# Optimization experiments

Measured on AMD Instinct MI355X. Metric: run time of the kernel, lower is better.

The kernel has to match this reference:

```python
import jax, jax.numpy as jnp
import numpy as np
from jax import lax

LATENT_DIM = 512
UNITS = LATENT_DIM // 2  # per-direction LSTM units (Keras LSTM(latent_dim//2))
FEAT = 512


def _lstm_scan(x, W, U, b):
    """Keras-style LSTM over x: [B, T, F]. Gate order i, f, g(candidate), o.
    Returns (hs [B,T,u], h_last [B,u], c_last [B,u])."""
    B = x.shape[0]
    u = U.shape[0]
    # Precompute input projections for all timesteps (one big GEMM).
    xz = jnp.einsum('btf,fg->btg', x, W) + b  # [B, T, 4u]

    def step(carry, zt):
        h, c = carry
        z = zt + h @ U  # [B, 4u]
        i = jax.nn.sigmoid(z[:, :u])
        f = jax.nn.sigmoid(z[:, u:2 * u])
        g = jnp.tanh(z[:, 2 * u:3 * u])
        o = jax.nn.sigmoid(z[:, 3 * u:])
        c_new = f * c + i * g
        h_new = o * jnp.tanh(c_new)
        return (h_new, c_new), h_new

    init = (jnp.zeros((B, u), x.dtype), jnp.zeros((B, u), x.dtype))
    (h_last, c_last), hs = lax.scan(step, init, jnp.swapaxes(xz, 0, 1))
    return jnp.swapaxes(hs, 0, 1), h_last, c_last


def setup_inputs() -> dict:
    key = jax.random.key(0)
    ks = jax.random.split(key, 7)
    B, T, F, u = 64, 1024, FEAT, UNITS
    s_in = 1.0 / np.sqrt(F)
    s_rec = 1.0 / np.sqrt(u)
    return {
        'x': jax.random.normal(ks[0], (B, T, F), jnp.float32),
        'W_fwd': jax.random.normal(ks[1], (F, 4 * u), jnp.float32) * s_in,
        'U_fwd': jax.random.normal(ks[2], (u, 4 * u), jnp.float32) * s_rec,
        'b_fwd': jnp.zeros((4 * u,), jnp.float32),
        'W_bwd': jax.random.normal(ks[3], (F, 4 * u), jnp.float32) * s_in,
        'U_bwd': jax.random.normal(ks[4], (u, 4 * u), jnp.float32) * s_rec,
        'b_bwd': jnp.zeros((4 * u,), jnp.float32),
    }


def reference(x, W_fwd, U_fwd, b_fwd, W_bwd, U_bwd, b_bwd):
    # Forward direction
    hs_f, h_f, c_f = _lstm_scan(x, W_fwd, U_fwd, b_fwd)
    # Backward direction: process reversed sequence, re-reverse outputs (Keras Bidirectional)
    hs_b, h_b, c_b = _lstm_scan(x[:, ::-1, :], W_bwd, U_bwd, b_bwd)
    hs_b = hs_b[:, ::-1, :]
    enc_out = jnp.concatenate([hs_f, hs_b], axis=-1)  # [B, T, latent]
    h = jnp.concatenate([h_f, h_b], axis=-1)          # [B, latent]
    c = jnp.concatenate([c_f, c_b], axis=-1)          # [B, latent]
    return enc_out, h, c
```

## Files before the change

kernel.cpp:

```cpp
#include <hip/hip_runtime.h>
#include <cstdint>
#include <cstddef>

typedef _Float16 f16x2 __attribute__((ext_vector_type(2)));
typedef _Float16 half4 __attribute__((ext_vector_type(4)));
typedef _Float16 half8 __attribute__((ext_vector_type(8)));
typedef float f32x4 __attribute__((ext_vector_type(4)));

static constexpr int BB = 64;
static constexpr int TT = 1024;
static constexpr int FF = 512;
static constexpr int UU = 256;
static constexpr int NZ = 1024;

static constexpr size_t LSTM_SHBYTES = 90112;

__device__ __forceinline__ f16x2 bc16(unsigned int v) { return __builtin_bit_cast(f16x2, v); }

__device__ __forceinline__ void st_u32_rlx(unsigned int* p, unsigned int v)
{
    __hip_atomic_store(p, v, __ATOMIC_RELAXED, __HIP_MEMORY_SCOPE_AGENT);
}
__device__ __forceinline__ unsigned int ld_u32_rlx(const unsigned int* p)
{
    return __hip_atomic_load(p, __ATOMIC_RELAXED, __HIP_MEMORY_SCOPE_AGENT);
}

__global__ __launch_bounds__(256) void enc_cast_x(
    const float* __restrict__ x, _Float16* __restrict__ x16, int n4)
{
    int stride = gridDim.x * 256;
    for (int i = blockIdx.x * 256 + threadIdx.x; i < n4; i += stride) {
        float4 v = ((const float4*)x)[i];
        half4 o;
        o.x = (_Float16)v.x; o.y = (_Float16)v.y;
        o.z = (_Float16)v.z; o.w = (_Float16)v.w;
        ((half4*)x16)[i] = o;
    }
}

__global__ __launch_bounds__(256) void enc_cast_wt(
    const float* __restrict__ Wf, const float* __restrict__ Wb,
    _Float16* __restrict__ WT)
{
    __shared__ float tile[64][65];
    const int t = threadIdx.x;
    const int k0 = blockIdx.x * 64;
    const int n0 = blockIdx.y * 64;
    const int d = blockIdx.z;
    const float* W = d ? Wb : Wf;
    _Float16* WTd = WT + (size_t)d * NZ * FF;
#pragma unroll
    for (int p = 0; p < 16; ++p) {
        int idx = p * 256 + t;
        int r = idx >> 6, c = idx & 63;
        tile[r][c] = W[(size_t)(k0 + r) * NZ + n0 + c];
    }
    __syncthreads();
#pragma unroll
    for (int p = 0; p < 16; ++p) {
        int idx = p * 256 + t;
        int r = idx >> 6, c = idx & 63;
        WTd[(size_t)(n0 + r) * FF + k0 + c] = (_Float16)tile[c][r];
    }
}

__global__ __launch_bounds__(256) void enc_pack_u16v2(
    const float* __restrict__ Uf, const float* __restrict__ Ub,
    uint4* __restrict__ Upkr2)
{
    int idx = blockIdx.x * 256 + threadIdx.x;
    if (idx >= 2 * 128 * 256) return;
    int d  = idx >> 15;
    int k2 = (idx >> 8) & 127;
    int j  = idx & 255;
    int k = 2 * k2;
    const float* Ud = d ? Ub : Uf;
    unsigned int w[4];
#pragma unroll
    for (int g = 0; g < 4; ++g) {
        f16x2 h;
        h.x = (_Float16)Ud[(size_t)k * NZ + g * 256 + j];
        h.y = (_Float16)Ud[(size_t)(k + 1) * NZ + g * 256 + j];
        w[g] = __builtin_bit_cast(unsigned int, h);
    }
    Upkr2[idx] = make_uint4(w[0], w[1], w[2], w[3]);
}

__global__ __launch_bounds__(256) void enc_zero(float* __restrict__ p, int n)
{
    int i = blockIdx.x * 256 + threadIdx.x;
    if (i < n) p[i] = 0.f;
}

__global__ __launch_bounds__(256) void enc_gemm16(
    const _Float16* __restrict__ x16, const _Float16* __restrict__ WT,
    const float* __restrict__ bf, const float* __restrict__ bb,
    _Float16* __restrict__ xz16, int c0, int CT)
{
    __shared__ __align__(16) _Float16 Ash[128][40];
    __shared__ __align__(16) _Float16 Bsh[128][40];

    const int t = threadIdx.x;
    const int r0 = blockIdx.x * 128;
    const int n0 = blockIdx.y * 128;
    const int MperD = BB * CT;
    const int d = r0 / MperD;

    const int srow = t >> 2;
    const int koff = (t & 3) * 8;

    auto xrowptr = [&](int r) -> const _Float16* {
        int rd = r - d * MperD;
        int b = rd / CT;
        int tl = rd - b * CT;
        int tsrc = d ? (TT - 1 - (c0 + tl)) : (c0 + tl);
        return x16 + ((size_t)b * TT + tsrc) * FF;
    };
    const _Float16* ap0 = xrowptr(r0 + srow);
    const _Float16* ap1 = xrowptr(r0 + 64 + srow);
    const _Float16* wp0 = WT + (size_t)(d * NZ + n0 + srow) * FF;
    const _Float16* wp1 = wp0 + (size_t)64 * FF;

    const int lane = t & 63;
    const int w = t >> 6;
    const int wm = w >> 1, wn = w & 1;
    const int l15 = lane & 15;
    const int kq = (lane >> 4) * 8;

    f32x4 acc[4][4];
#pragma unroll
    for (int i = 0; i < 4; ++i)
#pragma unroll
        for (int j = 0; j < 4; ++j) acc[i][j] = (f32x4)0.f;

    for (int ks = 0; ks < FF / 32; ++ks) {
        const int k0 = ks * 32;
        uint4 av0 = *(const uint4*)(ap0 + k0 + koff);
        uint4 av1 = *(const uint4*)(ap1 + k0 + koff);
        uint4 bv0 = *(const uint4*)(wp0 + k0 + koff);
        uint4 bv1 = *(const uint4*)(wp1 + k0 + koff);
        __syncthreads();
        *(uint4*)&Ash[srow][koff]      = av0;
        *(uint4*)&Ash[64 + srow][koff] = av1;
        *(uint4*)&Bsh[srow][koff]      = bv0;
        *(uint4*)&Bsh[64 + srow][koff] = bv1;
        __syncthreads();

        half8 af[4], bfr[4];
#pragma unroll
        for (int mf = 0; mf < 4; ++mf)
            af[mf] = *(const half8*)&Ash[wm * 64 + mf * 16 + l15][kq];
#pragma unroll
        for (int nf = 0; nf < 4; ++nf)
            bfr[nf] = *(const half8*)&Bsh[wn * 64 + nf * 16 + l15][kq];
#pragma unroll
        for (int mf = 0; mf < 4; ++mf)
#pragma unroll
            for (int nf = 0; nf < 4; ++nf)
                acc[mf][nf] = __builtin_amdgcn_mfma_f32_16x16x32_f16(
                    af[mf], bfr[nf], acc[mf][nf], 0, 0, 0);
    }

    const float* bd = d ? bb : bf;
    const int rbase = r0 + wm * 64;
    const int cbase = n0 + wn * 64;
#pragma unroll
    for (int nf = 0; nf < 4; ++nf) {
        const int cc = cbase + nf * 16 + l15;
        const float bia = bd[cc];
#pragma unroll
        for (int mf = 0; mf < 4; ++mf) {
#pragma unroll
            for (int rg = 0; rg < 4; ++rg) {
                int rr = rbase + mf * 16 + (lane >> 4) * 4 + rg;
                xz16[(size_t)rr * NZ + cc] = (_Float16)(acc[mf][nf][rg] + bia);
            }
        }
    }
}

__device__ __forceinline__ float sigm_f(float xv)
{
    return 1.0f / (1.0f + __expf(-xv));
}
__device__ __forceinline__ float tanh_f(float xv)
{
    return 2.0f / (1.0f + __expf(-2.0f * xv)) - 1.0f;
}

__global__ __launch_bounds__(512, 2) void enc_lstm_split(
    const _Float16* __restrict__ xz16, const uint4* __restrict__ Upkr2,
    float* __restrict__ hstate, float* __restrict__ cstate,
    unsigned int* __restrict__ hbuf,
    float* __restrict__ out, int c0, int CT)
{
    extern __shared__ char smem2[];
    float4*    parts = (float4*)smem2;
    _Float16*  hsh   = (_Float16*)(smem2 + 6144);
    uint4*     hshq  = (uint4*)hsh;

    const int t  = threadIdx.x;
    const int s  = t >> 7;
    const int jl = t & 127;
    const int beta = blockIdx.x;
    const int jh = (beta >> 3) & 1;
    const int c  = ((beta >> 4) << 3) | (beta & 7);
    const int d  = c >> 6;
    const int b  = c & 63;
    const int j  = jh * 128 + jl;
    const int partner = beta ^ 8;

    const uint4* Uq = Upkr2 + ((size_t)d * 128 + s * 32) * 256 + j;
    f16x2 ureg[32][4];
#pragma unroll
    for (int m = 0; m < 32; ++m) {
        uint4 qv = Uq[(size_t)m * 256];
        ureg[m][0] = bc16(qv.x);
        ureg[m][1] = bc16(qv.y);
        ureg[m][2] = bc16(qv.z);
        ureg[m][3] = bc16(qv.w);
    }

    float cr = 0.f, hn = 0.f;
    if (s == 0) cr = cstate[(size_t)c * UU + j];
    if (t < 256) hsh[t] = (_Float16)hstate[(size_t)c * UU + t];
    __syncthreads();

    const _Float16* xzrow = xz16 + (size_t)c * CT * NZ;
    float* outb = out + (size_t)b * TT * (2 * UU) + d * UU;

    for (int tl = 0; tl < CT; ++tl) {
        const int step = c0 + tl + 1;

        float x0 = 0.f, x1 = 0.f, x2 = 0.f, x3 = 0.f;
        if (s == 0) {
            const _Float16* p = xzrow + (size_t)tl * NZ + j;
            x0 = (float)p[0];   x1 = (float)p[256];
            x2 = (float)p[512]; x3 = (float)p[768];
        }

        float a0 = 0.f, a1 = 0.f, a2 = 0.f, a3 = 0.f;
#pragma unroll
        for (int r = 0; r < 8; ++r) {
            uint4 hq = hshq[s * 8 + r];
            f16x2 hw[4] = {bc16(hq.x), bc16(hq.y), bc16(hq.z), bc16(hq.w)};
#pragma unroll
            for (int q = 0; q < 4; ++q) {
                const int m = r * 4 + q;
                a0 = __builtin_amdgcn_fdot2(hw[q], ureg[m][0], a0, false);
                a1 = __builtin_amdgcn_fdot2(hw[q], ureg[m][1], a1, false);
                a2 = __builtin_amdgcn_fdot2(hw[q], ureg[m][2], a2, false);
                a3 = __builtin_amdgcn_fdot2(hw[q], ureg[m][3], a3, false);
            }
        }

        if (s) parts[(s - 1) * 128 + jl] = make_float4(a0, a1, a2, a3);
        __syncthreads();

        if (s == 0) {
            float4 p1 = parts[jl], p2 = parts[128 + jl], p3 = parts[256 + jl];
            float zi = a0 + p1.x + p2.x + p3.x + x0;
            float zf = a1 + p1.y + p2.y + p3.y + x1;
            float zg = a2 + p1.z + p2.z + p3.z + x2;
            float zo = a3 + p1.w + p2.w + p3.w + x3;
            float ig = sigm_f(zi), fg = sigm_f(zf), gg = tanh_f(zg), og = sigm_f(zo);
            cr = fg * cr + ig * gg;
            hn = og * tanh_f(cr);
            _Float16 h16 = (_Float16)hn;
            st_u32_rlx(&hbuf[((size_t)(step & 1) * 256 + beta) * 128 + jl],
                       ((unsigned int)step << 16)
                       | (unsigned int)__builtin_bit_cast(unsigned short, h16));
            hsh[j] = h16;
            int tsrc = d ? (TT - 1 - (c0 + tl)) : (c0 + tl);
            outb[(size_t)tsrc * (2 * UU) + j] = hn;
        }
        if (s == 1) {
            const unsigned int* p =
                &hbuf[((size_t)(step & 1) * 256 + partner) * 128 + jl];
            unsigned int v;
            do {
                v = ld_u32_rlx(p);
            } while ((v >> 16) != (unsigned int)step);
            hsh[(1 - jh) * 128 + jl] =
                __builtin_bit_cast(_Float16, (unsigned short)(v & 0xffffu));
        }
        __syncthreads();
    }

    if (s == 0) {
        hstate[(size_t)c * UU + j] = hn;
        cstate[(size_t)c * UU + j] = cr;
    }
}

__global__ __launch_bounds__(256) void enc_final(
    const float* __restrict__ hstate, const float* __restrict__ cstate,
    float* __restrict__ out)
{
    int idx = blockIdx.x * 256 + threadIdx.x;
    if (idx >= 2 * BB * UU) return;
    int d = idx / (BB * UU);
    int rem = idx - d * (BB * UU);
    int b = rem / UU;
    int j = rem - b * UU;
    size_t OUT_H = (size_t)BB * TT * (2 * UU);
    size_t HSZ = (size_t)BB * (2 * UU);
    out[OUT_H + (size_t)b * (2 * UU) + d * UU + j] = hstate[idx];
    out[OUT_H + HSZ + (size_t)b * (2 * UU) + d * UU + j] = cstate[idx];
}

extern "C" void kernel_launch(void* const* d_in, const int* in_sizes, int n_in,
                              void* d_out, int out_size, void* d_ws, size_t ws_size,
                              hipStream_t stream)
{
    const float* x  = (const float*)d_in[0];
    const float* Wf = (const float*)d_in[1];
    const float* Uf = (const float*)d_in[2];
    const float* bf = (const float*)d_in[3];
    const float* Wb = (const float*)d_in[4];
    const float* Ub = (const float*)d_in[5];
    const float* bb = (const float*)d_in[6];
    float* out = (float*)d_out;

    const size_t x16_bytes   = (size_t)BB * TT * FF * 2;
    const size_t wt_bytes    = (size_t)2 * NZ * FF * 2;
    const size_t upk_bytes   = (size_t)2 * 128 * 256 * sizeof(uint4);
    const size_t state_bytes = (size_t)2 * BB * UU * sizeof(float);
    const size_t hbuf_bytes  = (size_t)2 * 256 * 128 * 4;
    const size_t fixed = x16_bytes + wt_bytes + upk_bytes + 2 * state_bytes
                       + hbuf_bytes;

    int CT = TT;
    while (CT > 8) {
        size_t need = fixed + (size_t)2 * BB * CT * NZ * 2;
        if (need <= ws_size) break;
        CT >>= 1;
    }

    char* wsb = (char*)d_ws;
    _Float16* x16 = (_Float16*)wsb;
    _Float16* WT  = (_Float16*)(wsb + x16_bytes);
    uint4* Upkr2  = (uint4*)(wsb + x16_bytes + wt_bytes);
    float* hstate = (float*)(wsb + x16_bytes + wt_bytes + upk_bytes);
    float* cstate = hstate + 2 * BB * UU;
    unsigned int* hbuf = (unsigned int*)(wsb + x16_bytes + wt_bytes + upk_bytes
                                         + 2 * state_bytes);
    _Float16* xz16 = (_Float16*)(wsb + fixed);

    (void)hipFuncSetAttribute(reinterpret_cast<const void*>(enc_lstm_split),
                              hipFuncAttributeMaxDynamicSharedMemorySize,
                              (int)LSTM_SHBYTES);

    enc_cast_x<<<4096, 256, 0, stream>>>(x, x16, BB * TT * FF / 4);
    enc_cast_wt<<<dim3(8, 16, 2), 256, 0, stream>>>(Wf, Wb, WT);
    enc_pack_u16v2<<<(2 * 128 * 256 + 255) / 256, 256, 0, stream>>>(Uf, Ub, Upkr2);
    enc_zero<<<(2 * 2 * BB * UU + 255) / 256, 256, 0, stream>>>(hstate, 2 * 2 * BB * UU);

    for (int c0 = 0; c0 < TT; c0 += CT) {
        dim3 ggrid((2 * BB * CT) / 128, NZ / 128);
        enc_gemm16<<<ggrid, 256, 0, stream>>>(x16, WT, bf, bb, xz16, c0, CT);
        enc_lstm_split<<<256, 512, LSTM_SHBYTES, stream>>>(
            xz16, Upkr2, hstate, cstate, hbuf, out, c0, CT);
    }
    enc_final<<<(2 * BB * UU + 255) / 256, 256, 0, stream>>>(hstate, cstate, out);
}
```

Measured before the change: 1.878 ms.

## Overlap partner hidden-state exchange with local half of recurrent dot products

Restructures the per-step LSTM loop so the two waves that own the block's local h half compute their dot products while another wave waits for the partner block's h half, then the remaining waves finish the dot product. Each wave now writes its partial sums to shared memory and wave 0 reduces all four. The next timestep's xz inputs are prefetched, and the partner's flag word is loaded speculatively. Barriers become lightweight lgkmcnt waits, and the spin loop adds s_sleep. This adds a third barrier per step and depends on the relaxed-atomic handshake staying correct.

```diff
diff --git a/kernel.cpp b/kernel.cpp
--- a/kernel.cpp
+++ b/kernel.cpp
@@ -24,6 +24,11 @@
 __device__ __forceinline__ unsigned int ld_u32_rlx(const unsigned int* p)
 {
     return __hip_atomic_load(p, __ATOMIC_RELAXED, __HIP_MEMORY_SCOPE_AGENT);
+}
+
+__device__ __forceinline__ void bar_lgkm()
+{
+    asm volatile("s_waitcnt lgkmcnt(0)\n\ts_barrier" ::: "memory");
 }
 
 __global__ __launch_bounds__(256) void enc_cast_x(
@@ -197,7 +202,7 @@
 {
     extern __shared__ char smem2[];
     float4*    parts = (float4*)smem2;
-    _Float16*  hsh   = (_Float16*)(smem2 + 6144);
+    _Float16*  hsh   = (_Float16*)(smem2 + 8192);
     uint4*     hshq  = (uint4*)hsh;
 
     const int t  = threadIdx.x;
@@ -210,6 +215,8 @@
     const int b  = c & 63;
     const int j  = jh * 128 + jl;
     const int partner = beta ^ 8;
+    const bool own = ((s >> 1) == jh);
+    const bool isx = (s == (jh ? 1 : 2));
 
     const uint4* Uq = Upkr2 + ((size_t)d * 128 + s * 32) * 256 + j;
     f16x2 ureg[32][4];
@@ -230,17 +237,14 @@
     const _Float16* xzrow = xz16 + (size_t)c * CT * NZ;
     float* outb = out + (size_t)b * TT * (2 * UU) + d * UU;
 
-    for (int tl = 0; tl < CT; ++tl) {
-        const int step = c0 + tl + 1;
-
-        float x0 = 0.f, x1 = 0.f, x2 = 0.f, x3 = 0.f;
-        if (s == 0) {
-            const _Float16* p = xzrow + (size_t)tl * NZ + j;
-            x0 = (float)p[0];   x1 = (float)p[256];
-            x2 = (float)p[512]; x3 = (float)p[768];
-        }
-
-        float a0 = 0.f, a1 = 0.f, a2 = 0.f, a3 = 0.f;
+    unsigned short xp0 = 0, xp1 = 0, xp2 = 0, xp3 = 0;
+    if (s == 0) {
+        const unsigned short* p = (const unsigned short*)xzrow + j;
+        xp0 = p[0]; xp1 = p[256]; xp2 = p[512]; xp3 = p[768];
+    }
+    unsigned int pref = 0;
+
+    auto dot4 = [&](float& a0, float& a1, float& a2, float& a3) {
 #pragma unroll
         for (int r = 0; r < 8; ++r) {
             uint4 hq = hshq[s * 8 + r];
@@ -254,16 +258,48 @@
                 a3 = __builtin_amdgcn_fdot2(hw[q], ureg[m][3], a3, false);
             }
         }
-
-        if (s) parts[(s - 1) * 128 + jl] = make_float4(a0, a1, a2, a3);
-        __syncthreads();
+    };
+
+    for (int tl = 0; tl < CT; ++tl) {
+        const int step = c0 + tl + 1;
+        const int htag = c0 + tl;
+
+        if (own) {
+            float a0 = 0.f, a1 = 0.f, a2 = 0.f, a3 = 0.f;
+            dot4(a0, a1, a2, a3);
+            parts[s * 128 + jl] = make_float4(a0, a1, a2, a3);
+        }
+        if (isx && tl > 0) {
+            const unsigned int* pp =
+                &hbuf[((size_t)(htag & 1) * 256 + partner) * 128 + jl];
+            unsigned int v = pref;
+            while ((v >> 16) != (unsigned int)htag) {
+                __builtin_amdgcn_s_sleep(1);
+                v = ld_u32_rlx(pp);
+            }
+            hsh[(1 - jh) * 128 + jl] =
+                __builtin_bit_cast(_Float16, (unsigned short)(v & 0xffffu));
+        }
+        bar_lgkm();
+
+        if (!own) {
+            float a0 = 0.f, a1 = 0.f, a2 = 0.f, a3 = 0.f;
+            dot4(a0, a1, a2, a3);
+            parts[s * 128 + jl] = make_float4(a0, a1, a2, a3);
+        }
+        bar_lgkm();
 
         if (s == 0) {
-            float4 p1 = parts[jl], p2 = parts[128 + jl], p3 = parts[256 + jl];
-            float zi = a0 + p1.x + p2.x + p3.x + x0;
-            float zf = a1 + p1.y + p2.y + p3.y + x1;
-            float zg = a2 + p1.z + p2.z + p3.z + x2;
-            float zo = a3 + p1.w + p2.w + p3.w + x3;
+            float4 p0 = parts[jl], p1 = parts[128 + jl];
+            float4 p2 = parts[256 + jl], p3 = parts[384 + jl];
+            float zi = p0.x + p1.x + p2.x + p3.x
+                     + (float)__builtin_bit_cast(_Float16, xp0);
+            float zf = p0.y + p1.y + p2.y + p3.y
+                     + (float)__builtin_bit_cast(_Float16, xp1);
+            float zg = p0.z + p1.z + p2.z + p3.z
+                     + (float)__builtin_bit_cast(_Float16, xp2);
+            float zo = p0.w + p1.w + p2.w + p3.w
+                     + (float)__builtin_bit_cast(_Float16, xp3);
             float ig = sigm_f(zi), fg = sigm_f(zf), gg = tanh_f(zg), og = sigm_f(zo);
             cr = fg * cr + ig * gg;
             hn = og * tanh_f(cr);
@@ -274,18 +310,15 @@
             hsh[j] = h16;
             int tsrc = d ? (TT - 1 - (c0 + tl)) : (c0 + tl);
             outb[(size_t)tsrc * (2 * UU) + j] = hn;
-        }
-        if (s == 1) {
-            const unsigned int* p =
-                &hbuf[((size_t)(step & 1) * 256 + partner) * 128 + jl];
-            unsigned int v;
-            do {
-                v = ld_u32_rlx(p);
-            } while ((v >> 16) != (unsigned int)step);
-            hsh[(1 - jh) * 128 + jl] =
-                __builtin_bit_cast(_Float16, (unsigned short)(v & 0xffffu));
-        }
-        __syncthreads();
+            int tn = (tl + 1 < CT) ? tl + 1 : tl;
+            const unsigned short* pn =
+                (const unsigned short*)(xzrow + (size_t)tn * NZ) + j;
+            xp0 = pn[0]; xp1 = pn[256]; xp2 = pn[512]; xp3 = pn[768];
+        }
+        if (isx) {
+            pref = ld_u32_rlx(&hbuf[((size_t)(step & 1) * 256 + partner) * 128 + jl]);
+        }
+        bar_lgkm();
     }
 
     if (s == 0) {
```

New measurement: 1.697 ms. -9.6%, faster.
